# Kernel tuning notes

Measured on AMD Instinct MI355X. Metric: run time of the kernel, lower is better.

## Reference

```python
import jax, jax.numpy as jnp
import numpy as np

# FIR kernel from resample_kernel=(1,3,3,1): outer product, normalized (gain=1)
_FIR_1D = np.array([1.0, 3.0, 3.0, 1.0], dtype=np.float32)
_FIR = np.outer(_FIR_1D, _FIR_1D)
_FIR = _FIR / _FIR.sum()  # 4x4


def setup_inputs() -> dict:
    key = jax.random.key(0)
    k1, k2, k3 = jax.random.split(key, 3)
    x = jax.random.normal(k1, (16, 256, 64, 64), dtype=jnp.float32)
    # fan_avg uniform init (default_init): variance = 1/fan_avg, fan_in=fan_out=256*9
    scale = float(np.sqrt(3.0 / (256 * 9)))
    w = jax.random.uniform(k2, (256, 256, 3, 3), dtype=jnp.float32, minval=-scale, maxval=scale)
    b = jax.random.normal(k3, (256,), dtype=jnp.float32) * 0.01
    return {"x": x, "w": w, "b": b}


def reference(x, w, b):
    # conv_downsample_2d: upfirdn2d(x, k, pad=(2,2)) then conv2d stride 2, then + bias
    B, C, H, W = x.shape
    # upfirdn2d with up=1, down=1 == zero-padded true convolution with k.
    # k is symmetric so flip is a no-op, but keep it for faithfulness.
    fir = jnp.asarray(_FIR[::-1, ::-1])                       # [4,4]
    fir_k = jnp.tile(fir[None, None, :, :], (C, 1, 1, 1))     # [C,1,4,4] depthwise
    x = jax.lax.conv_general_dilated(
        x, fir_k,
        window_strides=(1, 1),
        padding=((2, 2), (2, 2)),                             # (p+1)//2, p//2 with p=4
        feature_group_count=C,
        dimension_numbers=("NCHW", "OIHW", "NCHW"),
    )                                                          # [B,C,H+1,W+1]
    y = jax.lax.conv_general_dilated(
        x, w,
        window_strides=(2, 2),
        padding="VALID",
        dimension_numbers=("NCHW", "OIHW", "NCHW"),
    )                                                          # [B,outC,H//2,W//2]
    return y + b[None, :, None, None]
```

## Files before the change

### kernel.cpp

```cpp
#include <hip/hip_runtime.h>
#include <hip/hip_bf16.h>

typedef __attribute__((ext_vector_type(8))) short bf16x8;
typedef __attribute__((ext_vector_type(4))) float f32x4;
typedef __attribute__((ext_vector_type(8))) unsigned short u16x8;

#define KD 2304
#define OUT_PER_B (256 * 1024)

static __device__ __forceinline__ ushort f2bf(float f) {
  union { float f; unsigned int i; } v; v.f = f;
  unsigned int x = v.i;
  x += 0x7fffu + ((x >> 16) & 1u);
  return (ushort)(x >> 16);
}
static __device__ __forceinline__ float bf2f(ushort u) {
  union { unsigned int i; float f; } v; v.i = ((unsigned)u) << 16; return v.f;
}

#define GLDS16(gp, lp)                                                         \
  __builtin_amdgcn_global_load_lds(                                            \
      (const __attribute__((address_space(1))) void*)(gp),                     \
      (__attribute__((address_space(3))) void*)(lp), 16, 0, 0)

#define SWZ(g, r) (((g) & 8) | (((g) ^ (r)) & 7))

__global__ __launch_bounds__(256) void k_fir4(const float* __restrict__ x,
                                              ushort* __restrict__ xft,
                                              const float* __restrict__ wsrc,
                                              ushort* __restrict__ wb) {
  __shared__ float sxAll[4][8 * 84];
  __shared__ ushort ringAll[4][4 * 65 * 8];
  const int band = blockIdx.x;
  const int cg = blockIdx.y;
  const int b = blockIdx.z;
  const int t = threadIdx.x;
  const int wid = t >> 6, lane = t & 63;
  const int coct = cg * 32 + wid * 8;
  const int r0 = band * 13;
  float* sx = sxAll[wid];
  ushort* ring = ringAll[wid];

  {
    int flat = band + 5 * (cg + 8 * b);
    for (int iw = flat * 256 + t; iw < 589824; iw += 163840) {
      float v = wsrc[iw];
      int j = iw % 9;
      int t2 = iw / 9;
      int ic = t2 & 255, oc = t2 >> 8;
      wb[oc * KD + j * 256 + ic] = f2bf(v);
    }
  }

  if (lane < 32) {
    int r = lane >> 2, cs = lane & 3;
    sx[r * 84 + (cs < 2 ? 2 + cs : 66 + cs)] = 0.f;
  }

  for (int it = 0; it < 17; ++it) {
    const int ir = r0 - 2 + it;

    float4 rg0, rg1;
    if (it <= 15) {
      if (ir >= 0 && ir < 64) {
        rg0 = *(const float4*)(x +
              ((size_t)((b * 256 + coct + (lane >> 4)) * 64 + ir) << 6) +
              (lane & 15) * 4);
        rg1 = *(const float4*)(x +
              ((size_t)((b * 256 + coct + 4 + (lane >> 4)) * 64 + ir) << 6) +
              (lane & 15) * 4);
      } else {
        rg0 = rg1 = make_float4(0.f, 0.f, 0.f, 0.f);
      }
    }

    if (it >= 4) {
      const int o = r0 - 4 + it;
      for (int w = lane; w < 65; w += 64) {
        u16x8 r4[4];
#pragma unroll
        for (int d = 0; d < 4; ++d) {
          int slot = (o - 2 + d) & 3;
          r4[d] = *(const u16x8*)&ring[(slot * 65 + w) * 8];
        }
        u16x8 ov;
#pragma unroll
        for (int k = 0; k < 8; ++k) {
          float f0 = bf2f(r4[0][k]), f1 = bf2f(r4[1][k]);
          float f2 = bf2f(r4[2][k]), f3 = bf2f(r4[3][k]);
          ov[k] = f2bf(((f0 + f3) + 3.f * (f1 + f2)) * 0.015625f);
        }
        *(u16x8*)&xft[((size_t)(b * 4225 + o * 65 + w) << 8) + coct] = ov;
      }
    }

    if (it <= 15) {
      *(float4*)&sx[(lane >> 4) * 84 + 4 + (lane & 15) * 4] = rg0;
      *(float4*)&sx[(4 + (lane >> 4)) * 84 + 4 + (lane & 15) * 4] = rg1;
    }
    __builtin_amdgcn_wave_barrier();

    if (it <= 15) {
      ushort* rw = ring + (ir & 3) * 65 * 8;
      for (int idx = lane; idx < 136; idx += 64) {
        int g = idx >> 3, c = idx & 7;
        const float* s = &sx[c * 84 + g * 4];
        float4 a0 = *(const float4*)(s);
        float4 a1 = *(const float4*)(s + 4);
        float4 a2 = *(const float4*)(s + 8);
        int w0 = g * 4;
        rw[w0 * 8 + c] = f2bf((a0.z + a1.y) + 3.f * (a0.w + a1.x));
        if (w0 + 1 < 65) rw[(w0 + 1) * 8 + c] = f2bf((a0.w + a1.z) + 3.f * (a1.x + a1.y));
        if (w0 + 2 < 65) rw[(w0 + 2) * 8 + c] = f2bf((a1.x + a1.w) + 3.f * (a1.y + a1.z));
        if (w0 + 3 < 65) rw[(w0 + 3) * 8 + c] = f2bf((a1.y + a2.x) + 3.f * (a1.z + a1.w));
      }
    }
    __builtin_amdgcn_wave_barrier();
  }
}

__global__ __launch_bounds__(256) void k_gemm3(const ushort* __restrict__ Wb,
                                               const ushort* __restrict__ Xt,
                                               const float* __restrict__ bias,
                                               float* __restrict__ out) {
  __shared__ ushort lA[128 * 128];
  __shared__ ushort lB[64 * 128];
  const int bid = blockIdx.x;
  const int work = (bid & 7) * 64 + (bid >> 3);
  const int ntile = work >> 1;
  const int mtile = work & 1;
  const int m0 = mtile * 128;
  const int n0 = ntile * 64;
  const int t = threadIdx.x;
  const int wid = t >> 6, lane = t & 63;
  const int wm = wid >> 1, wn = wid & 1;
  const int lrow = lane & 15, kgrp = lane >> 4;

  const ushort* aB[8];
#pragma unroll
  for (int i = 0; i < 8; ++i) {
    int idx = i * 256 + t;
    int row = idx >> 4, gL = idx & 15;
    aB[i] = Wb + (size_t)(m0 + row) * KD + SWZ(gL, row) * 8;
  }
  const ushort* bB[4];
#pragma unroll
  for (int i = 0; i < 4; ++i) {
    int idx = i * 256 + t;
    int row = idx >> 4, gL = idx & 15;
    int n = n0 + row;
    int b = n >> 10, oh = (n >> 5) & 31, ow = n & 31;
    bB[i] = Xt + ((size_t)((b * 65 + 2 * oh) * 65 + 2 * ow) << 8) +
            SWZ(gL, row) * 8;
  }

  f32x4 acc[4][2];
#pragma unroll
  for (int i = 0; i < 4; ++i)
#pragma unroll
    for (int j = 0; j < 2; ++j) acc[i][j] = (f32x4){0.f, 0.f, 0.f, 0.f};

  for (int kt = 0; kt < 18; ++kt) {
    const int j = kt >> 1;
    const int dh = j / 3, dw = j - 3 * dh;
    const int boff = (dh * 65 + dw) * 256 + ((kt & 1) << 7);
    const int k0 = kt << 7;
    __syncthreads();
#pragma unroll
    for (int i = 0; i < 8; ++i)
      GLDS16(aB[i] + k0, &lA[(i * 256 + t) * 8]);
#pragma unroll
    for (int i = 0; i < 4; ++i)
      GLDS16(bB[i] + boff, &lB[(i * 256 + t) * 8]);
    __syncthreads();

#pragma unroll
    for (int s = 0; s < 4; ++s) {
      bf16x8 Af[4], Bf[2];
#pragma unroll
      for (int f = 0; f < 4; ++f) {
        int row = wm * 64 + f * 16 + lrow;
        Af[f] = *(const bf16x8*)&lA[row * 128 + SWZ(s * 4 + kgrp, row) * 8];
      }
#pragma unroll
      for (int f = 0; f < 2; ++f) {
        int row = wn * 32 + f * 16 + lrow;
        Bf[f] = *(const bf16x8*)&lB[row * 128 + SWZ(s * 4 + kgrp, row) * 8];
      }
#pragma unroll
      for (int fm = 0; fm < 4; ++fm)
#pragma unroll
        for (int fn = 0; fn < 2; ++fn)
          acc[fm][fn] = __builtin_amdgcn_mfma_f32_16x16x32_bf16(
              Af[fm], Bf[fn], acc[fm][fn], 0, 0, 0);
    }
  }

  f32x4 bv[4];
#pragma unroll
  for (int fm = 0; fm < 4; ++fm)
    bv[fm] = *(const f32x4*)(bias + m0 + wm * 64 + fm * 16 + kgrp * 4);

#pragma unroll
  for (int fm = 0; fm < 4; ++fm) {
#pragma unroll
    for (int fn = 0; fn < 2; ++fn) {
      int nn = n0 + wn * 32 + fn * 16 + lrow;
      int oc = m0 + wm * 64 + fm * 16 + kgrp * 4;
      float* op = out + (size_t)(nn >> 10) * OUT_PER_B + (nn & 1023) +
                  (size_t)oc * 1024;
      op[0]    = acc[fm][fn][0] + bv[fm][0];
      op[1024] = acc[fm][fn][1] + bv[fm][1];
      op[2048] = acc[fm][fn][2] + bv[fm][2];
      op[3072] = acc[fm][fn][3] + bv[fm][3];
    }
  }
}

extern "C" void kernel_launch(void* const* d_in, const int* in_sizes, int n_in,
                              void* d_out, int out_size, void* d_ws, size_t ws_size,
                              hipStream_t stream) {
  const float* x    = (const float*)d_in[0];
  const float* w    = (const float*)d_in[1];
  const float* bias = (const float*)d_in[2];
  float* out = (float*)d_out;

  char* ws = (char*)d_ws;
  ushort* xft = (ushort*)ws;
  ushort* wb  = (ushort*)(ws + 34611200);

  k_fir4<<<dim3(5, 8, 16), 256, 0, stream>>>(x, xft, w, wb);
  k_gemm3<<<512, 256, 0, stream>>>(wb, xft, bias, out);
}
```

Before: 67.56 us.

## Rewrite FIR prepass to keep vertical taps in registers and shuffle horizontally

The FIR kernel now holds a rolling 8-row register window per lane and computes the vertical 1-3-3-1 pass in fp32 registers. The horizontal pass uses lane shuffles instead of LDS staging. This removes the intermediate bf16 rounding and the LDS ring buffer. Output is packed with v_cvt_pk_bf16_f32 and transposed through a small swizzled LDS stage for channel-last stores. Bands become 16 rows (the last band does 1), which changes work balance, and register use rises from the larger window.

New measurement: 61.48 us. -9.0%, faster.

```diff
diff --git a/kernel.cpp b/kernel.cpp
--- a/kernel.cpp
+++ b/kernel.cpp
@@ -14,9 +14,6 @@
   x += 0x7fffu + ((x >> 16) & 1u);
   return (ushort)(x >> 16);
 }
-static __device__ __forceinline__ float bf2f(ushort u) {
-  union { unsigned int i; float f; } v; v.i = ((unsigned)u) << 16; return v.f;
-}
 
 #define GLDS16(gp, lp)                                                         \
   __builtin_amdgcn_global_load_lds(                                            \
@@ -25,21 +22,24 @@
 
 #define SWZ(g, r) (((g) & 8) | (((g) ^ (r)) & 7))
 
-__global__ __launch_bounds__(256) void k_fir4(const float* __restrict__ x,
+#define CVTPK(d, lo, hi) \
+  asm("v_cvt_pk_bf16_f32 %0, %1, %2" : "=v"(d) : "v"(lo), "v"(hi))
+
+__global__ __launch_bounds__(256) void k_fir5(const float* __restrict__ x,
                                               ushort* __restrict__ xft,
                                               const float* __restrict__ wsrc,
                                               ushort* __restrict__ wb) {
-  __shared__ float sxAll[4][8 * 84];
-  __shared__ ushort ringAll[4][4 * 65 * 8];
+  __shared__ ushort stageAll[4][8 * 80];
   const int band = blockIdx.x;
   const int cg = blockIdx.y;
   const int b = blockIdx.z;
   const int t = threadIdx.x;
   const int wid = t >> 6, lane = t & 63;
-  const int coct = cg * 32 + wid * 8;
-  const int r0 = band * 13;
-  float* sx = sxAll[wid];
-  ushort* ring = ringAll[wid];
+  const int c = lane >> 3, o = lane & 7;
+  const int cw = cg * 32 + wid * 8;
+  const int h0 = band * 16;
+  const int nrows = (band == 4) ? 1 : 16;
+  ushort* stage = stageAll[wid];
 
   {
     int flat = band + 5 * (cg + 8 * b);
@@ -47,75 +47,86 @@
       float v = wsrc[iw];
       int j = iw % 9;
       int t2 = iw / 9;
-      int ic = t2 & 255, oc = t2 >> 8;
-      wb[oc * KD + j * 256 + ic] = f2bf(v);
-    }
-  }
-
-  if (lane < 32) {
-    int r = lane >> 2, cs = lane & 3;
-    sx[r * 84 + (cs < 2 ? 2 + cs : 66 + cs)] = 0.f;
-  }
-
-  for (int it = 0; it < 17; ++it) {
-    const int ir = r0 - 2 + it;
-
-    float4 rg0, rg1;
-    if (it <= 15) {
-      if (ir >= 0 && ir < 64) {
-        rg0 = *(const float4*)(x +
-              ((size_t)((b * 256 + coct + (lane >> 4)) * 64 + ir) << 6) +
-              (lane & 15) * 4);
-        rg1 = *(const float4*)(x +
-              ((size_t)((b * 256 + coct + 4 + (lane >> 4)) * 64 + ir) << 6) +
-              (lane & 15) * 4);
-      } else {
-        rg0 = rg1 = make_float4(0.f, 0.f, 0.f, 0.f);
+      wb[(t2 >> 8) * KD + j * 256 + (t2 & 255)] = f2bf(v);
+    }
+  }
+
+  const float* xrow = x + ((size_t)(b * 256 + cw + c) << 12) + o * 8;
+
+  float4 rA[8], rB[8];
+#define LOADR(s, r)                                                            \
+  {                                                                            \
+    if ((unsigned)(r) < 64u) {                                                 \
+      rA[s] = *(const float4*)(xrow + (r) * 64);                               \
+      rB[s] = *(const float4*)(xrow + (r) * 64 + 4);                           \
+    } else {                                                                   \
+      rA[s] = make_float4(0.f, 0.f, 0.f, 0.f);                                 \
+      rB[s] = make_float4(0.f, 0.f, 0.f, 0.f);                                 \
+    }                                                                          \
+  }
+
+  LOADR(6, h0 - 2)
+  LOADR(7, h0 - 1)
+  LOADR(0, h0)
+  LOADR(1, h0 + 1)
+  LOADR(2, h0 + 2)
+
+#pragma unroll
+  for (int hh = 0; hh < 16; ++hh) {
+    if (hh < nrows) {
+      const int h = h0 + hh;
+      LOADR((hh + 3) & 7, h + 3)
+
+      const int sm2 = (hh + 6) & 7, sm1 = (hh + 7) & 7;
+      const int s00 = hh & 7, sp1 = (hh + 1) & 7;
+      float v0 = (rA[sm2].x + rA[sp1].x) + 3.f * (rA[sm1].x + rA[s00].x);
+      float v1 = (rA[sm2].y + rA[sp1].y) + 3.f * (rA[sm1].y + rA[s00].y);
+      float v2 = (rA[sm2].z + rA[sp1].z) + 3.f * (rA[sm1].z + rA[s00].z);
+      float v3 = (rA[sm2].w + rA[sp1].w) + 3.f * (rA[sm1].w + rA[s00].w);
+      float v4 = (rB[sm2].x + rB[sp1].x) + 3.f * (rB[sm1].x + rB[s00].x);
+      float v5 = (rB[sm2].y + rB[sp1].y) + 3.f * (rB[sm1].y + rB[s00].y);
+      float v6 = (rB[sm2].z + rB[sp1].z) + 3.f * (rB[sm1].z + rB[s00].z);
+      float v7 = (rB[sm2].w + rB[sp1].w) + 3.f * (rB[sm1].w + rB[s00].w);
+
+      float vm1 = __shfl_up(v7, 1);
+      float vm2 = __shfl_up(v6, 1);
+      float vp  = __shfl_down(v0, 1);
+      if (o == 0) { vm1 = 0.f; vm2 = 0.f; }
+      if (o == 7) vp = 0.f;
+
+      const float S = 0.015625f;
+      float g0 = ((vm2 + v1) + 3.f * (vm1 + v0)) * S;
+      float g1 = ((vm1 + v2) + 3.f * (v0 + v1)) * S;
+      float g2 = ((v0 + v3) + 3.f * (v1 + v2)) * S;
+      float g3 = ((v1 + v4) + 3.f * (v2 + v3)) * S;
+      float g4 = ((v2 + v5) + 3.f * (v3 + v4)) * S;
+      float g5 = ((v3 + v6) + 3.f * (v4 + v5)) * S;
+      float g6 = ((v4 + v7) + 3.f * (v5 + v6)) * S;
+      float g7 = ((v5 + vp) + 3.f * (v6 + v7)) * S;
+
+      unsigned d0, d1, d2, d3;
+      CVTPK(d0, g0, g1);
+      CVTPK(d1, g2, g3);
+      CVTPK(d2, g4, g5);
+      CVTPK(d3, g6, g7);
+      *(uint4*)&stage[c * 80 + ((o ^ c) << 3)] = make_uint4(d0, d1, d2, d3);
+      if (o == 7)
+        stage[c * 80 + 64] = f2bf((v6 + 3.f * v7) * S);
+      __builtin_amdgcn_wave_barrier();
+
+      u16x8 pk;
+#pragma unroll
+      for (int cc = 0; cc < 8; ++cc)
+        pk[cc] = stage[cc * 80 + (((lane >> 3) ^ cc) << 3) + (lane & 7)];
+      *(u16x8*)&xft[((size_t)(b * 4225 + h * 65 + lane) << 8) + cw] = pk;
+      if (lane == 0) {
+        u16x8 p2;
+#pragma unroll
+        for (int cc = 0; cc < 8; ++cc) p2[cc] = stage[cc * 80 + 64];
+        *(u16x8*)&xft[((size_t)(b * 4225 + h * 65 + 64) << 8) + cw] = p2;
       }
-    }
-
-    if (it >= 4) {
-      const int o = r0 - 4 + it;
-      for (int w = lane; w < 65; w += 64) {
-        u16x8 r4[4];
-#pragma unroll
-        for (int d = 0; d < 4; ++d) {
-          int slot = (o - 2 + d) & 3;
-          r4[d] = *(const u16x8*)&ring[(slot * 65 + w) * 8];
-        }
-        u16x8 ov;
-#pragma unroll
-        for (int k = 0; k < 8; ++k) {
-          float f0 = bf2f(r4[0][k]), f1 = bf2f(r4[1][k]);
-          float f2 = bf2f(r4[2][k]), f3 = bf2f(r4[3][k]);
-          ov[k] = f2bf(((f0 + f3) + 3.f * (f1 + f2)) * 0.015625f);
-        }
-        *(u16x8*)&xft[((size_t)(b * 4225 + o * 65 + w) << 8) + coct] = ov;
-      }
-    }
-
-    if (it <= 15) {
-      *(float4*)&sx[(lane >> 4) * 84 + 4 + (lane & 15) * 4] = rg0;
-      *(float4*)&sx[(4 + (lane >> 4)) * 84 + 4 + (lane & 15) * 4] = rg1;
-    }
-    __builtin_amdgcn_wave_barrier();
-
-    if (it <= 15) {
-      ushort* rw = ring + (ir & 3) * 65 * 8;
-      for (int idx = lane; idx < 136; idx += 64) {
-        int g = idx >> 3, c = idx & 7;
-        const float* s = &sx[c * 84 + g * 4];
-        float4 a0 = *(const float4*)(s);
-        float4 a1 = *(const float4*)(s + 4);
-        float4 a2 = *(const float4*)(s + 8);
-        int w0 = g * 4;
-        rw[w0 * 8 + c] = f2bf((a0.z + a1.y) + 3.f * (a0.w + a1.x));
-        if (w0 + 1 < 65) rw[(w0 + 1) * 8 + c] = f2bf((a0.w + a1.z) + 3.f * (a1.x + a1.y));
-        if (w0 + 2 < 65) rw[(w0 + 2) * 8 + c] = f2bf((a1.x + a1.w) + 3.f * (a1.y + a1.z));
-        if (w0 + 3 < 65) rw[(w0 + 3) * 8 + c] = f2bf((a1.y + a2.x) + 3.f * (a1.z + a1.w));
-      }
-    }
-    __builtin_amdgcn_wave_barrier();
+      __builtin_amdgcn_wave_barrier();
+    }
   }
 }
 
@@ -229,6 +240,6 @@
   ushort* xft = (ushort*)ws;
   ushort* wb  = (ushort*)(ws + 34611200);
 
-  k_fir4<<<dim3(5, 8, 16), 256, 0, stream>>>(x, xft, w, wb);
+  k_fir5<<<dim3(5, 8, 16), 256, 0, stream>>>(x, xft, w, wb);
   k_gemm3<<<512, 256, 0, stream>>>(wb, xft, bias, out);
 }
```
